# Performance work log

Measured on AMD Instinct MI355X. Metric: run time of the kernel, lower is better.

Reference implementation:

```python
import jax, jax.numpy as jnp
import numpy as np

B, T, C_IN, DIM, NFFT, HOP = 8, 1024, 256, 512, 1024, 256
NOUT = NFFT // 2 + 1
BB_DIL = (1, 1, 2, 2, 4, 4, 8, 8)
RES_DIL = (1, 3, 5)
N_RES = 3


def conv1d(x, w, b, dilation=1, groups=1, padding=0):
    # x: (B,C,T), w: (O, I/groups, K)
    y = jax.lax.conv_general_dilated(
        x, w, window_strides=(1,), padding=[(padding, padding)],
        rhs_dilation=(dilation,), dimension_numbers=('NCH', 'OIH', 'NCH'),
        feature_group_count=groups)
    return y + b[None, :, None]


def layernorm(x, g, b, eps=1e-6):
    m = jnp.mean(x, -1, keepdims=True)
    v = jnp.mean((x - m) ** 2, -1, keepdims=True)
    return (x - m) * jax.lax.rsqrt(v + eps) * g + b


def istft(spec, window):
    # spec: (B, F, Tf) complex, center=True, hann window, win_length=n_fft
    Bsz, F_, Tf = spec.shape
    frames = jnp.fft.irfft(spec, n=NFFT, axis=1)            # (B, n_fft, Tf)
    frames = jnp.transpose(frames, (0, 2, 1)) * window       # (B, Tf, n_fft)
    L = NFFT + HOP * (Tf - 1)
    idx = jnp.arange(Tf)[:, None] * HOP + jnp.arange(NFFT)[None, :]  # (Tf, n_fft)
    y = jnp.zeros((Bsz, L), frames.dtype).at[:, idx].add(frames)
    env = jnp.zeros((L,), window.dtype).at[idx].add(
        jnp.broadcast_to(window ** 2, (Tf, NFFT)))
    y = y / jnp.where(env > 1e-11, env, 1.0)
    start = NFFT // 2
    return y[:, start:start + HOP * (Tf - 1)]


def setup_inputs() -> dict:
    key = jax.random.key(0)
    ks = iter(jax.random.split(key, 64))
    r = lambda *s: jax.random.normal(next(ks), s, jnp.float32) * 0.02
    return {
        'x': jax.random.normal(next(ks), (B, T, C_IN), jnp.float32),
        'conv_in_w': r(DIM, C_IN, 7), 'conv_in_b': r(DIM),
        'skip_w': r(DIM, C_IN, 1), 'skip_b': r(DIM),
        'bb_dw_w': r(8, DIM, 1, 7), 'bb_dw_b': r(8, DIM),
        'bb_ln_g': jnp.ones((8, DIM), jnp.float32), 'bb_ln_b': jnp.zeros((8, DIM), jnp.float32),
        'bb_pw1_w': r(8, 4 * DIM, DIM), 'bb_pw1_b': r(8, 4 * DIM),
        'bb_pw2_w': r(8, DIM, 4 * DIM), 'bb_pw2_b': r(8, DIM),
        'bb_gamma': jnp.full((8, DIM), 1e-6, jnp.float32),
        'res_w1': r(N_RES, 3, DIM, DIM, 3), 'res_b1': r(N_RES, 3, DIM),
        'res_w2': r(N_RES, 3, DIM, DIM, 3), 'res_b2': r(N_RES, 3, DIM),
        'ln_g': jnp.ones((DIM,), jnp.float32), 'ln_b': jnp.zeros((DIM,), jnp.float32),
        'mag_w1': r(DIM, DIM), 'mag_b1': r(DIM),
        'mag_w2': r(NOUT, DIM), 'mag_b2': r(NOUT),
        'ph_w': r(NOUT, DIM), 'ph_b': r(NOUT),
        'cumsum_w': jnp.linspace(0.05, 0.4, NOUT, dtype=jnp.float32)[None, :],
        'window': (0.5 - 0.5 * jnp.cos(2.0 * jnp.pi * jnp.arange(NFFT) / NFFT)).astype(jnp.float32),
    }


def reference(x, conv_in_w, conv_in_b, skip_w, skip_b,
              bb_dw_w, bb_dw_b, bb_ln_g, bb_ln_b,
              bb_pw1_w, bb_pw1_b, bb_pw2_w, bb_pw2_b, bb_gamma,
              res_w1, res_b1, res_w2, res_b2,
              ln_g, ln_b, mag_w1, mag_b1, mag_w2, mag_b2,
              ph_w, ph_b, cumsum_w, window):
    # (B,T,C) -> (B,C,T)
    h = jnp.transpose(x, (0, 2, 1))
    skip = conv1d(h, skip_w, skip_b)                     # (B,DIM,T)
    hp = jnp.pad(h, ((0, 0), (0, 0), (3, 3)), mode='reflect')
    h = conv1d(hp, conv_in_w, conv_in_b)                 # kernel 7, pad 0 -> (B,DIM,T)
    # ConvNeXt backbone
    for i, d in enumerate(BB_DIL):
        res = h
        pad = (7 + (d - 1) * 6) // 2
        y = conv1d(h, bb_dw_w[i], bb_dw_b[i], dilation=d, groups=DIM, padding=pad)
        y = jnp.transpose(y, (0, 2, 1))                  # (B,T,DIM)
        y = layernorm(y, bb_ln_g[i], bb_ln_b[i])
        y = jax.nn.gelu(y @ bb_pw1_w[i].T + bb_pw1_b[i], approximate=False)
        y = y @ bb_pw2_w[i].T + bb_pw2_b[i]
        y = bb_gamma[i] * y
        h = res + jnp.transpose(y, (0, 2, 1))
    h = h + skip                                         # same length T
    # Residual dilated conv stacks
    for i in range(N_RES):
        for j, d in enumerate(RES_DIL):
            y = conv1d(h, res_w1[i, j], res_b1[i, j], dilation=d, padding=d)
            y = jax.nn.leaky_relu(y, 0.1)
            y = conv1d(y, res_w2[i, j], res_b2[i, j], padding=1)
            h = h + y
    h = jnp.transpose(h, (0, 2, 1))                      # (B,T,DIM)
    h = layernorm(h, ln_g, ln_b)
    # magnitude head
    m = jax.nn.gelu(h @ mag_w1.T + mag_b1, approximate=False)
    log_mag = m @ mag_w2.T + mag_b2
    mag = jnp.exp(jnp.clip(log_mag, -10.0, 10.0))        # (B,T,NOUT)
    # instantaneous-frequency phase head
    inst = jnp.tanh(h @ ph_w.T + ph_b) * jnp.pi
    phase = jnp.cumsum(inst * cumsum_w, axis=1)
    phase = jnp.remainder(phase + jnp.pi, 2.0 * jnp.pi) - jnp.pi
    # synthesize
    spec = jax.lax.complex(mag * jnp.cos(phase), mag * jnp.sin(phase))
    spec = jnp.transpose(spec, (0, 2, 1))                # (B,F,T)
    return istft(spec, window)
```

## Files before the change

kernel.cpp:

```cpp
#include <hip/hip_runtime.h>
#include <math.h>

constexpr int Bv = 8, Tv = 1024, DIMC = 512, NOUTC = 513;
constexpr int Mrows = Bv * 1024;
constexpr int LDS_S = 1056;
constexpr float PI_F = 3.14159265358979323846f;
constexpr float TWOPI_F = 6.28318530717958647692f;

struct TapInfo { int n; int off[7]; };
struct PtrTable { _Float16* h[36]; };

enum { BND_NONE = 0, BND_ZERO, BND_REFLECT };

typedef _Float16 half8v __attribute__((ext_vector_type(8)));
typedef _Float16 half4v __attribute__((ext_vector_type(4)));
typedef float f32x4 __attribute__((ext_vector_type(4)));

__device__ __forceinline__ void gld_lds16(const void* g, void* l) {
  __builtin_amdgcn_global_load_lds(
      (const __attribute__((address_space(1))) unsigned int*)g,
      (__attribute__((address_space(3))) unsigned int*)l, 16, 0, 0);
}

enum { MEPI_GELU_H = 0, MEPI_GAMMARES };

template<int EPI, int TN, int KS>
__global__ __launch_bounds__(256)
void mfma_gemm(const _Float16* __restrict__ A, int lda,
               const _Float16* __restrict__ W, int K,
               const float* __restrict__ bias,
               const float* __restrict__ aux,
               float* __restrict__ hio,
               _Float16* __restrict__ Ch,
               int N, int ldc)
{
  constexpr int NFR = TN / 32;
  __shared__ _Float16 sA[2][KS * 128 * 32];
  __shared__ _Float16 sB[2][KS * TN * 32];
  const int m0 = blockIdx.x * 128;
  const int n0 = blockIdx.y * TN;
  const int tid = threadIdx.x;
  const int wid = tid >> 6, lane = tid & 63;
  const int wr = wid >> 1, wc = wid & 1;
  const int fr = lane & 15, fq = lane >> 4;

  f32x4 acc[4][NFR] = {};

  const int rbase = tid >> 2;
  const int kwS = (((tid & 3) ^ ((tid >> 3) & 3)) << 3);
  const int nst = K / (32 * KS);
  const int fqS = fq ^ ((fr >> 1) & 3);
  const int aBase = (wr * 64 + fr) * 32 + fqS * 8;
  const int bBase = (wc * (TN / 2) + fr) * 32 + fqS * 8;

  const _Float16* arow[2];
  #pragma unroll
  for (int s = 0; s < 2; ++s)
    arow[s] = A + (size_t)(m0 + s * 64 + rbase) * lda + kwS;

  auto STAGE = [&](int st, int buf) {
    #pragma unroll
    for (int ks = 0; ks < KS; ++ks) {
      const int k0 = (st * KS + ks) << 5;
      #pragma unroll
      for (int s = 0; s < 2; ++s)
        gld_lds16(arow[s] + k0,
                  (char*)&sA[buf][0] + ks * 8192 + s * 4096 + wid * 1024);
      #pragma unroll
      for (int s = 0; s < TN / 64; ++s) {
        size_t bo = (size_t)(n0 + s * 64 + rbase) * K + kwS + k0;
        gld_lds16(W + bo,
                  (char*)&sB[buf][0] + ks * (TN * 64) + s * 4096 + wid * 1024);
      }
    }
  };
  auto COMPUTE = [&](int buf) {
    #pragma unroll
    for (int ks = 0; ks < KS; ++ks) {
      half8v aF[4], bF[NFR];
      #pragma unroll
      for (int i = 0; i < 4; ++i)
        aF[i] = *(const half8v*)&sA[buf][ks * 4096 + aBase + i * 512];
      #pragma unroll
      for (int j = 0; j < NFR; ++j)
        bF[j] = *(const half8v*)&sB[buf][ks * (TN * 32) + bBase + j * 512];
      #pragma unroll
      for (int i = 0; i < 4; ++i)
        #pragma unroll
        for (int j = 0; j < NFR; ++j)
          acc[i][j] = __builtin_amdgcn_mfma_f32_16x16x32_f16(aF[i], bF[j], acc[i][j], 0, 0, 0);
    }
  };

  STAGE(0, 0);
  __syncthreads();
  int cur = 0;
  for (int st = 0; st < nst; ++st) {
    if (st + 1 < nst) STAGE(st + 1, cur ^ 1);
    COMPUTE(cur);
    __syncthreads();
    cur ^= 1;
  }

  #pragma unroll
  for (int j = 0; j < NFR; ++j) {
    const int n = n0 + wc * (TN / 2) + j * 16 + fr;
    const float bj = bias[n];
    const float gj = (EPI == MEPI_GAMMARES) ? aux[n] : 0.f;
    #pragma unroll
    for (int i = 0; i < 4; ++i) {
      const int mB = m0 + wr * 64 + i * 16 + fq * 4;
      #pragma unroll
      for (int r = 0; r < 4; ++r) {
        const int m = mB + r;
        float v = acc[i][j][r] + bj;
        if (EPI == MEPI_GELU_H) {
          v = 0.5f * v * (1.f + erff(v * 0.70710678118654752f));
          Ch[(size_t)m * ldc + n] = (_Float16)v;
        } else {
          hio[(size_t)m * ldc + n] += gj * v;
        }
      }
    }
  }
}

enum { SEPI_F32 = 0, SEPI_LEAKY_SPLIT, SEPI_ADDRES_SPLIT,
       SEPI_GELU_SPLIT, SEPI_EXPCLIP, SEPI_TANHCW };

template<int EPI, int BND, int TN>
__global__ __launch_bounds__(256)
void mfma_gemm_split(const _Float16* __restrict__ Ah, const _Float16* __restrict__ Al, int lda,
                     const _Float16* __restrict__ Wh, const _Float16* __restrict__ Wl, int K,
                     const float* __restrict__ bias,
                     const float* __restrict__ aux,
                     float* __restrict__ hio,
                     float* __restrict__ Cf,
                     _Float16* __restrict__ Chh, _Float16* __restrict__ Chl,
                     int N, int ldc,
                     const _Float16* __restrict__ zpage,
                     TapInfo taps)
{
  constexpr int NFR = TN / 32;
  __shared__ _Float16 sAh[2][128 * 32];
  __shared__ _Float16 sAl[2][128 * 32];
  __shared__ _Float16 sBh[2][TN * 32];
  __shared__ _Float16 sBl[2][TN * 32];
  const int m0 = blockIdx.x * 128;
  const int n0 = blockIdx.y * TN;
  const int tid = threadIdx.x;
  const int wid = tid >> 6, lane = tid & 63;
  const int wr = wid >> 1, wc = wid & 1;
  const int fr = lane & 15, fq = lane >> 4;

  f32x4 acc[4][NFR] = {};

  const int t0 = m0 & (Tv - 1);
  const int rbase = tid >> 2;
  const int kwS = (((tid & 3) ^ ((tid >> 3) & 3)) << 3);
  const int nkc = K >> 5;
  const int NT = taps.n * nkc;
  const int fqS = fq ^ ((fr >> 1) & 3);
  const int aBase = (wr * 64 + fr) * 32 + fqS * 8;
  const int bBase = (wc * (TN / 2) + fr) * 32 + fqS * 8;

  auto STAGE = [&](int st, int buf) {
    int tap = (taps.n == 1) ? 0 : (st / nkc);
    int kc = st - tap * nkc;
    const int k0 = kc << 5;
    const int off = (BND == BND_NONE) ? 0 : taps.off[tap];
    const _Float16* Wth = Wh + (size_t)tap * N * K;
    const _Float16* Wtl = Wl + (size_t)tap * N * K;
    #pragma unroll
    for (int s = 0; s < 2; ++s) {
      int t = t0 + s * 64 + rbase + off;
      bool valid = true;
      if (BND == BND_REFLECT) t = (t < 0) ? -t : (t >= Tv ? 2 * Tv - 2 - t : t);
      else if (BND == BND_ZERO) valid = (t >= 0) && (t < Tv);
      size_t ro = (size_t)(m0 - t0 + t) * lda + kwS + k0;
      const void* sh = valid ? (const void*)(Ah + ro) : (const void*)zpage;
      const void* sl = valid ? (const void*)(Al + ro) : (const void*)zpage;
      gld_lds16(sh, (char*)&sAh[buf][0] + s * 4096 + wid * 1024);
      gld_lds16(sl, (char*)&sAl[buf][0] + s * 4096 + wid * 1024);
    }
    #pragma unroll
    for (int s = 0; s < TN / 64; ++s) {
      size_t bo = (size_t)(n0 + s * 64 + rbase) * K + kwS + k0;
      gld_lds16(Wth + bo, (char*)&sBh[buf][0] + s * 4096 + wid * 1024);
      gld_lds16(Wtl + bo, (char*)&sBl[buf][0] + s * 4096 + wid * 1024);
    }
  };

  auto COMPUTE = [&](int buf) {
    half8v ah[4], al[4], bh[NFR], bl[NFR];
    #pragma unroll
    for (int i = 0; i < 4; ++i) {
      ah[i] = *(const half8v*)&sAh[buf][aBase + i * 512];
      al[i] = *(const half8v*)&sAl[buf][aBase + i * 512];
    }
    #pragma unroll
    for (int j = 0; j < NFR; ++j) {
      bh[j] = *(const half8v*)&sBh[buf][bBase + j * 512];
      bl[j] = *(const half8v*)&sBl[buf][bBase + j * 512];
    }
    #pragma unroll
    for (int i = 0; i < 4; ++i)
      #pragma unroll
      for (int j = 0; j < NFR; ++j) {
        acc[i][j] = __builtin_amdgcn_mfma_f32_16x16x32_f16(ah[i], bh[j], acc[i][j], 0, 0, 0);
        acc[i][j] = __builtin_amdgcn_mfma_f32_16x16x32_f16(ah[i], bl[j], acc[i][j], 0, 0, 0);
        acc[i][j] = __builtin_amdgcn_mfma_f32_16x16x32_f16(al[i], bh[j], acc[i][j], 0, 0, 0);
      }
  };

  STAGE(0, 0);
  __syncthreads();
  int cur = 0;
  for (int st = 0; st < NT; ++st) {
    if (st + 1 < NT) STAGE(st + 1, cur ^ 1);
    COMPUTE(cur);
    __syncthreads();
    cur ^= 1;
  }

  #pragma unroll
  for (int j = 0; j < NFR; ++j) {
    const int n = n0 + wc * (TN / 2) + j * 16 + fr;
    const bool nok = (n < N);
    const float bj = (nok && bias) ? bias[n] : 0.f;
    const float ax = (EPI == SEPI_TANHCW && nok) ? aux[n] : 0.f;
    #pragma unroll
    for (int i = 0; i < 4; ++i) {
      const int mB = m0 + wr * 64 + i * 16 + fq * 4;
      #pragma unroll
      for (int r = 0; r < 4; ++r) {
        const int m = mB + r;
        float v = acc[i][j][r] + bj;
        if (!nok) continue;
        if (EPI == SEPI_F32) {
          Cf[(size_t)m * ldc + n] = v;
        } else if (EPI == SEPI_GELU_SPLIT) {
          v = 0.5f * v * (1.f + erff(v * 0.70710678118654752f));
          _Float16 hi = (_Float16)v;
          Chh[(size_t)m * ldc + n] = hi;
          Chl[(size_t)m * ldc + n] = (_Float16)(v - (float)hi);
        } else if (EPI == SEPI_EXPCLIP) {
          Cf[(size_t)m * ldc + n] = expf(fminf(fmaxf(v, -10.f), 10.f));
        } else if (EPI == SEPI_TANHCW) {
          Cf[(size_t)m * ldc + n] = tanhf(v) * PI_F * ax;
        }
      }
    }
  }
}

enum { REPI_LEAKY = 0, REPI_ADDRES };

template<int EPI>
__global__ __launch_bounds__(256)
void res_gemm(const _Float16* __restrict__ Ah, const _Float16* __restrict__ Al,
              const _Float16* __restrict__ Wh, const _Float16* __restrict__ Wl,
              const float* __restrict__ bias,
              float* __restrict__ hio,
              _Float16* __restrict__ Chh, _Float16* __restrict__ Chl,
              const _Float16* __restrict__ zpage,
              int d)
{
  __shared__ _Float16 sAh_[160 * 32];
  __shared__ _Float16 sAl_[160 * 32];
  __shared__ _Float16 sB_[3 * 2 * 64 * 32];
  const int m0 = blockIdx.x * 128;
  const int n0 = blockIdx.y * 64;
  const int tid = threadIdx.x;
  const int wid = tid >> 6, lane = tid & 63;
  const int wr = wid >> 1, wc = wid & 1;
  const int fr = lane & 15, fq = lane >> 4;
  const int t0 = m0 & (Tv - 1);

  f32x4 acc[4][2] = {};
  const int offs[3] = {-d, 0, d};

  for (int kc = 0; kc < 16; ++kc) {
    const int k0h = kc << 5;
    #pragma unroll
    for (int it = 0; it < 5; ++it) {
      int cb = it * 4 + wid;
      int half = (cb >= 10) ? 1 : 0;
      int rb = (cb - half * 10) * 16;
      int row = rb + (lane >> 2);
      int slot_g = (lane & 3) ^ ((row >> 1) & 3);
      int t = t0 - 16 + row;
      bool valid = (t >= 0) && (t < Tv);
      const _Float16* srcb = half ? Al : Ah;
      const void* src = valid
          ? (const void*)(srcb + (size_t)(m0 - t0 + t) * DIMC + k0h + slot_g * 8)
          : (const void*)(zpage + slot_g * 8);
      void* dst = (char*)(half ? sAl_ : sAh_) + rb * 64;
      gld_lds16(src, dst);
    }
    #pragma unroll
    for (int it = 0; it < 6; ++it) {
      int cb = it * 4 + wid;
      int tap = cb >> 3;
      int r2 = cb & 7;
      int half = r2 >> 2;
      int rb = (r2 & 3) * 16;
      int row = rb + (lane >> 2);
      int slot_g = (lane & 3) ^ ((row >> 1) & 3);
      const _Float16* srcb = (half ? Wl : Wh) + (size_t)tap * 512 * 512
                           + (size_t)(n0 + row) * 512 + k0h + slot_g * 8;
      void* dst = (char*)sB_ + ((size_t)(tap * 2 + half) * 64 + rb) * 64;
      gld_lds16(srcb, dst);
    }
    __syncthreads();

    #pragma unroll
    for (int tap = 0; tap < 3; ++tap) {
      const int off = offs[tap];
      half8v ah[4], al[4], bh[2], bl[2];
      #pragma unroll
      for (int i = 0; i < 4; ++i) {
        int rA = wr * 64 + i * 16 + fr + off + 16;
        int ab = rA * 64 + ((fq ^ ((rA >> 1) & 3)) * 16);
        ah[i] = *(const half8v*)((const char*)sAh_ + ab);
        al[i] = *(const half8v*)((const char*)sAl_ + ab);
      }
      #pragma unroll
      for (int j = 0; j < 2; ++j) {
        int rB = wc * 32 + j * 16 + fr;
        int bb = rB * 64 + ((fq ^ ((rB >> 1) & 3)) * 16);
        bh[j] = *(const half8v*)((const char*)sB_ + (tap * 2 + 0) * 4096 + bb);
        bl[j] = *(const half8v*)((const char*)sB_ + (tap * 2 + 1) * 4096 + bb);
      }
      #pragma unroll
      for (int i = 0; i < 4; ++i)
        #pragma unroll
        for (int j = 0; j < 2; ++j) {
          acc[i][j] = __builtin_amdgcn_mfma_f32_16x16x32_f16(ah[i], bh[j], acc[i][j], 0, 0, 0);
          acc[i][j] = __builtin_amdgcn_mfma_f32_16x16x32_f16(ah[i], bl[j], acc[i][j], 0, 0, 0);
          acc[i][j] = __builtin_amdgcn_mfma_f32_16x16x32_f16(al[i], bh[j], acc[i][j], 0, 0, 0);
        }
    }
    __syncthreads();
  }

  #pragma unroll
  for (int j = 0; j < 2; ++j) {
    const int n = n0 + wc * 32 + j * 16 + fr;
    const float bj = bias[n];
    #pragma unroll
    for (int i = 0; i < 4; ++i) {
      const int mB = m0 + wr * 64 + i * 16 + fq * 4;
      #pragma unroll
      for (int r = 0; r < 4; ++r) {
        const int m = mB + r;
        float v = acc[i][j][r] + bj;
        if (EPI == REPI_LEAKY) {
          v = (v > 0.f) ? v : 0.1f * v;
          _Float16 hi = (_Float16)v;
          Chh[(size_t)m * DIMC + n] = hi;
          Chl[(size_t)m * DIMC + n] = (_Float16)(v - (float)hi);
        } else {
          float nh = hio[(size_t)m * DIMC + n] + v;
          hio[(size_t)m * DIMC + n] = nh;
          _Float16 hi = (_Float16)nh;
          Chh[(size_t)m * DIMC + n] = hi;
          Chl[(size_t)m * DIMC + n] = (_Float16)(nh - (float)hi);
        }
      }
    }
  }
}

__global__ __launch_bounds__(256)
void convin_gemm(const _Float16* __restrict__ Ah, const _Float16* __restrict__ Al,
                 const _Float16* __restrict__ Wh, const _Float16* __restrict__ Wl,
                 const float* __restrict__ bias,
                 float* __restrict__ Cf)
{
  __shared__ _Float16 sAh_[160 * 32];
  __shared__ _Float16 sAl_[160 * 32];
  __shared__ _Float16 sB_[7 * 2 * 64 * 32];
  const int m0 = blockIdx.x * 128;
  const int n0 = blockIdx.y * 64;
  const int tid = threadIdx.x;
  const int wid = tid >> 6, lane = tid & 63;
  const int wr = wid >> 1, wc = wid & 1;
  const int fr = lane & 15, fq = lane >> 4;
  const int t0 = m0 & (Tv - 1);

  f32x4 acc[4][2] = {};

  for (int kc = 0; kc < 8; ++kc) {
    const int k0h = kc << 5;
    #pragma unroll
    for (int it = 0; it < 5; ++it) {
      int cb = it * 4 + wid;
      int half = (cb >= 10) ? 1 : 0;
      int rb = (cb - half * 10) * 16;
      int row = rb + (lane >> 2);
      int slot_g = (lane & 3) ^ ((row >> 1) & 3);
      int t = t0 - 16 + row;
      t = (t < 0) ? -t : (t >= Tv ? 2 * Tv - 2 - t : t);
      const _Float16* srcb = half ? Al : Ah;
      const void* src = srcb + (size_t)(m0 - t0 + t) * 256 + k0h + slot_g * 8;
      void* dst = (char*)(half ? sAl_ : sAh_) + rb * 64;
      gld_lds16(src, dst);
    }
    #pragma unroll
    for (int it = 0; it < 14; ++it) {
      int cb = it * 4 + wid;
      int tap = cb >> 3;
      int r2 = cb & 7;
      int half = r2 >> 2;
      int rb = (r2 & 3) * 16;
      int row = rb + (lane >> 2);
      int slot_g = (lane & 3) ^ ((row >> 1) & 3);
      const _Float16* srcb = (half ? Wl : Wh) + (size_t)tap * 512 * 256
                           + (size_t)(n0 + row) * 256 + k0h + slot_g * 8;
      void* dst = (char*)sB_ + ((size_t)(tap * 2 + half) * 64 + rb) * 64;
      gld_lds16(srcb, dst);
    }
    __syncthreads();

    #pragma unroll
    for (int tap = 0; tap < 7; ++tap) {
      const int off = tap - 3;
      half8v ah[4], al[4], bh[2], bl[2];
      #pragma unroll
      for (int i = 0; i < 4; ++i) {
        int rA = wr * 64 + i * 16 + fr + off + 16;
        int ab = rA * 64 + ((fq ^ ((rA >> 1) & 3)) * 16);
        ah[i] = *(const half8v*)((const char*)sAh_ + ab);
        al[i] = *(const half8v*)((const char*)sAl_ + ab);
      }
      #pragma unroll
      for (int j = 0; j < 2; ++j) {
        int rB = wc * 32 + j * 16 + fr;
        int bb = rB * 64 + ((fq ^ ((rB >> 1) & 3)) * 16);
        bh[j] = *(const half8v*)((const char*)sB_ + (tap * 2 + 0) * 4096 + bb);
        bl[j] = *(const half8v*)((const char*)sB_ + (tap * 2 + 1) * 4096 + bb);
      }
      #pragma unroll
      for (int i = 0; i < 4; ++i)
        #pragma unroll
        for (int j = 0; j < 2; ++j) {
          acc[i][j] = __builtin_amdgcn_mfma_f32_16x16x32_f16(ah[i], bh[j], acc[i][j], 0, 0, 0);
          acc[i][j] = __builtin_amdgcn_mfma_f32_16x16x32_f16(ah[i], bl[j], acc[i][j], 0, 0, 0);
          acc[i][j] = __builtin_amdgcn_mfma_f32_16x16x32_f16(al[i], bh[j], acc[i][j], 0, 0, 0);
        }
    }
    __syncthreads();
  }

  #pragma unroll
  for (int j = 0; j < 2; ++j) {
    const int n = n0 + wc * 32 + j * 16 + fr;
    const float bj = bias[n];
    #pragma unroll
    for (int i = 0; i < 4; ++i) {
      const int mB = m0 + wr * 64 + i * 16 + fq * 4;
      #pragma unroll
      for (int r = 0; r < 4; ++r) {
        const int m = mB + r;
        Cf[(size_t)m * DIMC + n] = acc[i][j][r] + bj;
      }
    }
  }
}

__global__ __launch_bounds__(256)
void dwln(const float* __restrict__ h, const float* __restrict__ wt,
          const float* __restrict__ bias, const float* __restrict__ g,
          const float* __restrict__ be, _Float16* __restrict__ out, int d)
{
  int wid = threadIdx.x >> 6, lane = threadIdx.x & 63;
  int m = (blockIdx.x << 2) + wid;
  int t = m & (Tv - 1);
  int bT = m - t;
  int c0 = lane * 8;
  float acc[8];
  {
    float4 b0 = *(const float4*)&bias[c0];
    float4 b1 = *(const float4*)&bias[c0 + 4];
    acc[0] = b0.x; acc[1] = b0.y; acc[2] = b0.z; acc[3] = b0.w;
    acc[4] = b1.x; acc[5] = b1.y; acc[6] = b1.z; acc[7] = b1.w;
  }
  #pragma unroll
  for (int k = 0; k < 7; ++k) {
    int tt = t + (k - 3) * d;
    if (tt < 0 || tt >= Tv) continue;
    const float* hp = &h[(size_t)(bT + tt) * DIMC + c0];
    float4 v0 = *(const float4*)hp;
    float4 v1 = *(const float4*)(hp + 4);
    const float* wp = &wt[k * DIMC + c0];
    float4 w0 = *(const float4*)wp;
    float4 w1 = *(const float4*)(wp + 4);
    float hv[8] = {v0.x, v0.y, v0.z, v0.w, v1.x, v1.y, v1.z, v1.w};
    float wv[8] = {w0.x, w0.y, w0.z, w0.w, w1.x, w1.y, w1.z, w1.w};
    #pragma unroll
    for (int q = 0; q < 8; ++q)
      acc[q] = fmaf(hv[q], wv[q], acc[q]);
  }
  float sum = 0.f;
  #pragma unroll
  for (int q = 0; q < 8; ++q) sum += acc[q];
  #pragma unroll
  for (int o = 32; o > 0; o >>= 1) sum += __shfl_xor(sum, o);
  float mean = sum * (1.f / 512.f);
  float vs = 0.f;
  #pragma unroll
  for (int q = 0; q < 8; ++q) { float dd = acc[q] - mean; vs = fmaf(dd, dd, vs); }
  #pragma unroll
  for (int o = 32; o > 0; o >>= 1) vs += __shfl_xor(vs, o);
  float rstd = rsqrtf(vs * (1.f / 512.f) + 1e-6f);
  float4 g0 = *(const float4*)&g[c0];
  float4 g1 = *(const float4*)&g[c0 + 4];
  float4 e0 = *(const float4*)&be[c0];
  float4 e1 = *(const float4*)&be[c0 + 4];
  float gv[8] = {g0.x, g0.y, g0.z, g0.w, g1.x, g1.y, g1.z, g1.w};
  float ev[8] = {e0.x, e0.y, e0.z, e0.w, e1.x, e1.y, e1.z, e1.w};
  half8v ov;
  #pragma unroll
  for (int q = 0; q < 8; ++q)
    ov[q] = (_Float16)((acc[q] - mean) * rstd * gv[q] + ev[q]);
  *(half8v*)&out[(size_t)m * DIMC + c0] = ov;
}

__global__ __launch_bounds__(256)
void repack_dw(const float* __restrict__ in, float* __restrict__ out)
{
  int idx = blockIdx.x * 256 + threadIdx.x;
  if (idx >= 8 * 512 * 7) return;
  int l = idx / 3584;
  int r = idx - l * 3584;
  int c = r / 7, k = r - c * 7;
  out[l * 3584 + k * 512 + c] = in[idx];
}

__global__ __launch_bounds__(256)
void lnorm_split(const float* __restrict__ in, const float* __restrict__ g,
                 const float* __restrict__ be,
                 _Float16* __restrict__ ohi, _Float16* __restrict__ olo)
{
  int wid = threadIdx.x >> 6, lane = threadIdx.x & 63;
  int m = (blockIdx.x << 2) + wid;
  int c0 = lane * 8;
  const float* row = in + (size_t)m * DIMC + c0;
  float4 v0 = *(const float4*)row;
  float4 v1 = *(const float4*)(row + 4);
  float acc[8] = {v0.x, v0.y, v0.z, v0.w, v1.x, v1.y, v1.z, v1.w};
  float sum = 0.f;
  #pragma unroll
  for (int q = 0; q < 8; ++q) sum += acc[q];
  #pragma unroll
  for (int o = 32; o > 0; o >>= 1) sum += __shfl_xor(sum, o);
  float mean = sum * (1.f / 512.f);
  float vs = 0.f;
  #pragma unroll
  for (int q = 0; q < 8; ++q) { float dd = acc[q] - mean; vs = fmaf(dd, dd, vs); }
  #pragma unroll
  for (int o = 32; o > 0; o >>= 1) vs += __shfl_xor(vs, o);
  float rstd = rsqrtf(vs * (1.f / 512.f) + 1e-6f);
  float4 g0 = *(const float4*)&g[c0];
  float4 g1 = *(const float4*)&g[c0 + 4];
  float4 e0 = *(const float4*)&be[c0];
  float4 e1 = *(const float4*)&be[c0 + 4];
  float gv[8] = {g0.x, g0.y, g0.z, g0.w, g1.x, g1.y, g1.z, g1.w};
  float ev[8] = {e0.x, e0.y, e0.z, e0.w, e1.x, e1.y, e1.z, e1.w};
  half8v hv, lv;
  #pragma unroll
  for (int q = 0; q < 8; ++q) {
    float v = (acc[q] - mean) * rstd * gv[q] + ev[q];
    _Float16 hi = (_Float16)v;
    hv[q] = hi; lv[q] = (_Float16)(v - (float)hi);
  }
  *(half8v*)&ohi[(size_t)m * DIMC + c0] = hv;
  *(half8v*)&olo[(size_t)m * DIMC + c0] = lv;
}

__global__ __launch_bounds__(256)
void add_split(float* __restrict__ a, const float* __restrict__ b,
               _Float16* __restrict__ hi, _Float16* __restrict__ lo, int n)
{
  int i = (blockIdx.x * 256 + threadIdx.x) * 4;
  if (i >= n) return;
  float4 va = *(const float4*)&a[i];
  float4 vb = *(const float4*)&b[i];
  float v[4] = {va.x + vb.x, va.y + vb.y, va.z + vb.z, va.w + vb.w};
  *(float4*)&a[i] = make_float4(v[0], v[1], v[2], v[3]);
  half4v h, l;
  #pragma unroll
  for (int q = 0; q < 4; ++q) {
    _Float16 hh = (_Float16)v[q];
    h[q] = hh; l[q] = (_Float16)(v[q] - (float)hh);
  }
  *(half4v*)&hi[i] = h;
  *(half4v*)&lo[i] = l;
}

__global__ __launch_bounds__(256)
void cvt_split(const float* __restrict__ in, _Float16* __restrict__ hi,
               _Float16* __restrict__ lo, int n)
{
  int i = (blockIdx.x * 256 + threadIdx.x) * 4;
  if (i >= n) return;
  float4 vv = *(const float4*)&in[i];
  float v[4] = {vv.x, vv.y, vv.z, vv.w};
  half4v h, l;
  #pragma unroll
  for (int q = 0; q < 4; ++q) {
    _Float16 hh = (_Float16)v[q];
    h[q] = hh; l[q] = (_Float16)(v[q] - (float)hh);
  }
  *(half4v*)&hi[i] = h;
  *(half4v*)&lo[i] = l;
}

__global__ __launch_bounds__(256)
void cvt_split_pad(const float* __restrict__ in, _Float16* __restrict__ hi,
                   _Float16* __restrict__ lo, int rows, int cols, int padRows)
{
  int i = blockIdx.x * 256 + threadIdx.x;
  if (i >= padRows * cols) return;
  int r = i / cols;
  float v = (r < rows) ? in[i] : 0.f;
  _Float16 h = (_Float16)v;
  hi[i] = h; lo[i] = (_Float16)(v - (float)h);
}

__global__ __launch_bounds__(256)
void cvt_h(const float* __restrict__ in, _Float16* __restrict__ out, int n)
{
  int i = (blockIdx.x * 256 + threadIdx.x) * 4;
  if (i >= n) return;
  float4 v = *(const float4*)&in[i];
  half4v h;
  h[0] = (_Float16)v.x; h[1] = (_Float16)v.y;
  h[2] = (_Float16)v.z; h[3] = (_Float16)v.w;
  *(half4v*)&out[i] = h;
}

__global__ __launch_bounds__(256)
void repack_split(const float* __restrict__ in, _Float16* __restrict__ hi,
                  _Float16* __restrict__ lo, int O, int C, int KT)
{
  int idx = blockIdx.x * 256 + threadIdx.x;
  if (idx >= O * C) return;
  int o = idx / C, c = idx - o * C;
  for (int k = 0; k < KT; ++k) {
    float v = in[((size_t)o * C + c) * KT + k];
    _Float16 h = (_Float16)v;
    size_t dst = ((size_t)k * O + o) * C + c;
    hi[dst] = h; lo[dst] = (_Float16)(v - (float)h);
  }
}

__global__ __launch_bounds__(256)
void repack_all(const float* __restrict__ res_w1, const float* __restrict__ res_w2,
                PtrTable pt)
{
  int blk = blockIdx.x;
  int conv = blk >> 10;
  int idx = ((blk & 1023) << 8) + threadIdx.x;
  int o = idx >> 9, c = idx & 511;
  const float* src = (conv < 9) ? (res_w1 + (size_t)conv * 786432)
                                : (res_w2 + (size_t)(conv - 9) * 786432);
  _Float16* hi = pt.h[conv * 2];
  _Float16* lo = pt.h[conv * 2 + 1];
  #pragma unroll
  for (int k = 0; k < 3; ++k) {
    float v = src[((size_t)o * 512 + c) * 3 + k];
    _Float16 hh = (_Float16)v;
    size_t dst = ((size_t)k * 512 + o) * 512 + c;
    hi[dst] = hh; lo[dst] = (_Float16)(v - (float)hh);
  }
}

__global__ __launch_bounds__(256)
void zero_fill16(_Float16* __restrict__ p)
{
  int i = threadIdx.x * 8;
  #pragma unroll
  for (int q = 0; q < 8; ++q) p[i + q] = (_Float16)0.f;
}

__global__ __launch_bounds__(256)
void build_basis_split(const float* __restrict__ window,
                       _Float16* __restrict__ bhi, _Float16* __restrict__ blo)
{
  int n = blockIdx.x;
  float wn = window[n];
  const float invN = 1.f / 1024.f;
  for (int j = threadIdx.x; j < LDS_S; j += 256) {
    float coef = 0.f;
    if (j < 513) {
      int k = j;
      if (k == 0)        coef = invN;
      else if (k == 512) coef = (n & 1) ? -invN : invN;
      else {
        int r = (k * n) & 1023;
        coef = 2.f * invN * cosf(TWOPI_F * (float)r * (1.f / 1024.f));
      }
    } else if (j < 1026) {
      int k = j - 513;
      if (k != 0 && k != 512) {
        int r = (k * n) & 1023;
        coef = -2.f * invN * sinf(TWOPI_F * (float)r * (1.f / 1024.f));
      }
    }
    float v = coef * wn;
    _Float16 hi = (_Float16)v;
    bhi[(size_t)n * LDS_S + j] = hi;
    blo[(size_t)n * LDS_S + j] = (_Float16)(v - (float)hi);
  }
}

__global__ __launch_bounds__(256)
void scan_part(const float* __restrict__ dph, float* __restrict__ psum)
{
  int b = blockIdx.x, fg = blockIdx.y;
  int w = threadIdx.x >> 6, lane = threadIdx.x & 63;
  int tc = blockIdx.z * 4 + w;
  int f = fg * 64 + lane;
  if (f >= NOUTC) return;
  const float* p = dph + (size_t)(b * Tv + tc * 32) * NOUTC + f;
  float s = 0.f;
  #pragma unroll 8
  for (int j = 0; j < 32; ++j) s += p[(size_t)j * NOUTC];
  psum[((size_t)b * 32 + tc) * 520 + f] = s;
}

__global__ __launch_bounds__(256)
void scan_off(float* __restrict__ psum)
{
  int idx = blockIdx.x * 256 + threadIdx.x;
  if (idx >= 8 * NOUTC) return;
  int b = idx / NOUTC, f = idx - b * NOUTC;
  float run = 0.f;
  for (int tc = 0; tc < 32; ++tc) {
    size_t o = ((size_t)b * 32 + tc) * 520 + f;
    float v = psum[o];
    psum[o] = run;
    run += v;
  }
}

__global__ __launch_bounds__(256)
void scan_emit(const float* __restrict__ dph, const float* __restrict__ mag,
               const float* __restrict__ psum,
               _Float16* __restrict__ Shi, _Float16* __restrict__ Slo)
{
  int b = blockIdx.x, fg = blockIdx.y;
  int w = threadIdx.x >> 6, lane = threadIdx.x & 63;
  int tc = blockIdx.z * 4 + w;
  int f = fg * 64 + lane;
  if (f >= NOUTC) return;
  float run = psum[((size_t)b * 32 + tc) * 520 + f];
  const size_t base = (size_t)(b * Tv + tc * 32) * NOUTC + f;
  for (int j = 0; j < 32; ++j) {
    run += dph[base + (size_t)j * NOUTC];
    float r = fmodf(run + PI_F, TWOPI_F);
    if (r < 0.f) r += TWOPI_F;
    float wph = r - PI_F;
    float mg = mag[base + (size_t)j * NOUTC];
    float sn, cs;
    sincosf(wph, &sn, &cs);
    size_t mrow = (size_t)(b * Tv + tc * 32 + j) * LDS_S;
    float vc = mg * cs, vs2 = mg * sn;
    _Float16 hc = (_Float16)vc, hs = (_Float16)vs2;
    Shi[mrow + f] = hc;        Slo[mrow + f] = (_Float16)(vc - (float)hc);
    Shi[mrow + 513 + f] = hs;  Slo[mrow + 513 + f] = (_Float16)(vs2 - (float)hs);
  }
}

__global__ __launch_bounds__(256)
void pad_S(_Float16* __restrict__ Shi, _Float16* __restrict__ Slo)
{
  int idx = blockIdx.x * 256 + threadIdx.x;
  if (idx >= Mrows * 30) return;
  int m = idx / 30, c = 1026 + idx % 30;
  Shi[(size_t)m * LDS_S + c] = (_Float16)0.f;
  Slo[(size_t)m * LDS_S + c] = (_Float16)0.f;
}

__global__ __launch_bounds__(256)
void ola(const float* __restrict__ frames, const float* __restrict__ window,
         float* __restrict__ out)
{
  int idx = blockIdx.x * 256 + threadIdx.x;
  if (idx >= Bv * 261888) return;
  int b = idx / 261888;
  int i = idx - b * 261888;
  int l = i + 512;
  int tmax = l >> 8; if (tmax > 1023) tmax = 1023;
  int tmin = (l >= 1023) ? ((l - 1023 + 255) >> 8) : 0;
  float acc = 0.f, env = 0.f;
  for (int t = tmin; t <= tmax; ++t) {
    int n = l - (t << 8);
    acc += frames[(size_t)(b * Tv + t) * 1024 + n];
    float wv = window[n];
    env = fmaf(wv, wv, env);
  }
  out[idx] = acc / (env > 1e-11f ? env : 1.f);
}

extern "C" void kernel_launch(void* const* d_in, const int* in_sizes, int n_in,
                              void* d_out, int out_size, void* d_ws, size_t ws_size,
                              hipStream_t stream)
{
  const float* x         = (const float*)d_in[0];
  const float* conv_in_w = (const float*)d_in[1];
  const float* conv_in_b = (const float*)d_in[2];
  const float* skip_w    = (const float*)d_in[3];
  const float* skip_b    = (const float*)d_in[4];
  const float* bb_dw_w   = (const float*)d_in[5];
  const float* bb_dw_b   = (const float*)d_in[6];
  const float* bb_ln_g   = (const float*)d_in[7];
  const float* bb_ln_b   = (const float*)d_in[8];
  const float* bb_pw1_w  = (const float*)d_in[9];
  const float* bb_pw1_b  = (const float*)d_in[10];
  const float* bb_pw2_w  = (const float*)d_in[11];
  const float* bb_pw2_b  = (const float*)d_in[12];
  const float* bb_gamma  = (const float*)d_in[13];
  const float* res_w1    = (const float*)d_in[14];
  const float* res_b1    = (const float*)d_in[15];
  const float* res_w2    = (const float*)d_in[16];
  const float* res_b2    = (const float*)d_in[17];
  const float* ln_g      = (const float*)d_in[18];
  const float* ln_b      = (const float*)d_in[19];
  const float* mag_w1    = (const float*)d_in[20];
  const float* mag_b1    = (const float*)d_in[21];
  const float* mag_w2    = (const float*)d_in[22];
  const float* mag_b2    = (const float*)d_in[23];
  const float* ph_w      = (const float*)d_in[24];
  const float* ph_b      = (const float*)d_in[25];
  const float* cumsum_w  = (const float*)d_in[26];
  const float* window    = (const float*)d_in[27];
  float* out = (float*)d_out;
  float* ws  = (float*)d_ws;

  float* w_h     = ws;
  float* w_skip  = ws + 4194304;
  float* w_t4    = ws + 8388608;
  float* w_mag   = ws + 12582912;
  float* w_dph   = ws + 16785408;
  float* w_basis = ws + 20987904;
  float* w_big   = ws + 22069248;
  _Float16* t3h  = (_Float16*)w_big;
  _Float16* h_hi = (_Float16*)w_big;
  _Float16* h_lo = h_hi + 4194304;
  _Float16* y_hi = h_hi + 8388608;
  _Float16* y_lo = h_hi + 12582912;
  _Float16* Shi  = (_Float16*)w_big;
  _Float16* Slo  = Shi + 8650752;
  float* w_frames= w_h;

  _Float16* t2h  = (_Float16*)(ws + 30720000);
  _Float16* x_hi = (_Float16*)(ws + 32817152);
  _Float16* x_lo = (_Float16*)(ws + 33865728);
  _Float16* wA_hi= (_Float16*)(ws + 34914304);
  _Float16* wA_lo= (_Float16*)(ws + 35438592);
  _Float16* wB_hi= (_Float16*)(ws + 35962880);
  _Float16* wB_lo= (_Float16*)(ws + 36487168);
  _Float16* zpg  = (_Float16*)(ws + 37011456);
  float* w_psum  = ws + 37012480;
  float* w_dwT   = ws + 37145600;

  _Float16* wpw1h = (_Float16*)w_t4;
  _Float16* wpw2h = (_Float16*)w_mag;

  static const size_t slotOffF[18] = {
    8388608, 9175040, 9961472, 10747904, 11534336,
    12582912, 13369344, 14155776, 14942208, 15728640,
    16785408, 17571840, 18358272, 19144704, 19931136,
    32817152, 33603584,
    30720000
  };
  PtrTable pt;
  for (int cv = 0; cv < 18; ++cv) {
    _Float16* hi = (_Float16*)(ws + slotOffF[cv]);
    pt.h[cv * 2] = hi;
    pt.h[cv * 2 + 1] = hi + 786432;
  }

  _Float16* lshi = (_Float16*)w_skip;
  _Float16* lslo = lshi + 4194304;
  _Float16* t4hi = (_Float16*)w_t4;
  _Float16* t4lo = t4hi + 4194304;
  _Float16* m1hi = t2h;
  _Float16* m1lo = t2h + 262144;
  _Float16* m2hi = t2h + 524288;
  _Float16* m2lo = t2h + 851968;
  _Float16* phhi = t2h + 1179648;
  _Float16* phlo = t2h + 1507328;
  _Float16* bhi  = (_Float16*)w_basis;
  _Float16* blo  = bhi + 1081344;

  dim3 blk(256);
  TapInfo tp1{1, {0}};

  zero_fill16<<<dim3(1), blk, 0, stream>>>(zpg);
  cvt_split<<<dim3(8192 * 256 / 4 / 256), blk, 0, stream>>>(x, x_hi, x_lo, 8192 * 256);
  cvt_h<<<dim3(8388608 / 4 / 256), blk, 0, stream>>>(bb_pw1_w, wpw1h, 8388608);
  cvt_h<<<dim3(8388608 / 4 / 256), blk, 0, stream>>>(bb_pw2_w, wpw2h, 8388608);
  repack_dw<<<dim3(112), blk, 0, stream>>>(bb_dw_w, w_dwT);

  repack_split<<<dim3(512 * 256 / 256), blk, 0, stream>>>(conv_in_w, wA_hi, wA_lo, 512, 256, 7);
  convin_gemm<<<dim3(64, 8), blk, 0, stream>>>(
      x_hi, x_lo, wA_hi, wA_lo, conv_in_b, w_h);
  repack_split<<<dim3(512 * 256 / 256), blk, 0, stream>>>(skip_w, wB_hi, wB_lo, 512, 256, 1);
  mfma_gemm_split<SEPI_F32, BND_NONE, 64><<<dim3(64, 8), blk, 0, stream>>>(
      x_hi, x_lo, 256, wB_hi, wB_lo, 256, skip_b, nullptr, nullptr, w_skip, nullptr, nullptr,
      512, 512, zpg, tp1);

  const int dil[8] = {1, 1, 2, 2, 4, 4, 8, 8};
  for (int i = 0; i < 8; ++i) {
    dwln<<<dim3(2048), blk, 0, stream>>>(w_h, w_dwT + i * 3584, bb_dw_b + i * 512,
                                         bb_ln_g + i * 512, bb_ln_b + i * 512, t2h, dil[i]);
    mfma_gemm<MEPI_GELU_H, 128, 1><<<dim3(64, 16), blk, 0, stream>>>(
        t2h, 512, wpw1h + (size_t)i * 2048 * 512, 512, bb_pw1_b + i * 2048,
        nullptr, nullptr, t3h, 2048, 2048);
    mfma_gemm<MEPI_GAMMARES, 64, 2><<<dim3(64, 8), blk, 0, stream>>>(
        t3h, 2048, wpw2h + (size_t)i * 512 * 2048, 2048, bb_pw2_b + i * 512,
        bb_gamma + i * 512, w_h, nullptr, 512, 512);
  }
  add_split<<<dim3(4194304 / 4 / 256), blk, 0, stream>>>(w_h, w_skip, h_hi, h_lo, 4194304);

  repack_all<<<dim3(18 * 1024), blk, 0, stream>>>(res_w1, res_w2, pt);

  const int rdil[3] = {1, 3, 5};
  for (int i = 0; i < 3; ++i)
    for (int j = 0; j < 3; ++j) {
      int d = rdil[j];
      int idx = i * 3 + j;
      res_gemm<REPI_LEAKY><<<dim3(64, 8), blk, 0, stream>>>(
          h_hi, h_lo, pt.h[idx * 2], pt.h[idx * 2 + 1],
          res_b1 + idx * 512, nullptr, y_hi, y_lo, zpg, d);
      res_gemm<REPI_ADDRES><<<dim3(64, 8), blk, 0, stream>>>(
          y_hi, y_lo, pt.h[(9 + idx) * 2], pt.h[(9 + idx) * 2 + 1],
          res_b2 + idx * 512, w_h, h_hi, h_lo, zpg, 1);
    }

  lnorm_split<<<dim3(2048), blk, 0, stream>>>(w_h, ln_g, ln_b, lshi, lslo);

  cvt_split<<<dim3(262144 / 4 / 256), blk, 0, stream>>>(mag_w1, m1hi, m1lo, 262144);
  cvt_split_pad<<<dim3(640 * 512 / 256), blk, 0, stream>>>(mag_w2, m2hi, m2lo, 513, 512, 640);
  cvt_split_pad<<<dim3(640 * 512 / 256), blk, 0, stream>>>(ph_w, phhi, phlo, 513, 512, 640);

  mfma_gemm_split<SEPI_GELU_SPLIT, BND_NONE, 64><<<dim3(64, 8), blk, 0, stream>>>(
      lshi, lslo, 512, m1hi, m1lo, 512, mag_b1, nullptr, nullptr, nullptr,
      t4hi, t4lo, 512, 512, zpg, tp1);
  mfma_gemm_split<SEPI_EXPCLIP, BND_NONE, 64><<<dim3(64, 10), blk, 0, stream>>>(
      t4hi, t4lo, 512, m2hi, m2lo, 512, mag_b2, nullptr, nullptr, w_mag,
      nullptr, nullptr, 513, 513, zpg, tp1);
  mfma_gemm_split<SEPI_TANHCW, BND_NONE, 64><<<dim3(64, 10), blk, 0, stream>>>(
      lshi, lslo, 512, phhi, phlo, 512, ph_b, cumsum_w, nullptr, w_dph,
      nullptr, nullptr, 513, 513, zpg, tp1);

  build_basis_split<<<dim3(1024), blk, 0, stream>>>(window, bhi, blo);
  pad_S<<<dim3((Mrows * 30 + 255) / 256), blk, 0, stream>>>(Shi, Slo);
  scan_part<<<dim3(8, 9, 8), blk, 0, stream>>>(w_dph, w_psum);
  scan_off<<<dim3(17), blk, 0, stream>>>(w_psum);
  scan_emit<<<dim3(8, 9, 8), blk, 0, stream>>>(w_dph, w_mag, w_psum, Shi, Slo);
  mfma_gemm_split<SEPI_F32, BND_NONE, 128><<<dim3(64, 8), blk, 0, stream>>>(
      Shi, Slo, LDS_S, bhi, blo, LDS_S, nullptr, nullptr, nullptr, w_frames,
      nullptr, nullptr, 1024, 1024, zpg, tp1);
  ola<<<dim3((Bv * 261888 + 255) / 256), blk, 0, stream>>>(w_frames, window, out);
}
```

Before: 1.839 ms.

## Double-buffer res_gemm LDS staging and keep residual only as fp16 hi/lo

```diff
diff --git a/kernel.cpp b/kernel.cpp
--- a/kernel.cpp
+++ b/kernel.cpp
@@ -261,14 +261,15 @@
 void res_gemm(const _Float16* __restrict__ Ah, const _Float16* __restrict__ Al,
               const _Float16* __restrict__ Wh, const _Float16* __restrict__ Wl,
               const float* __restrict__ bias,
-              float* __restrict__ hio,
+              const _Float16* __restrict__ prevHi,
+              const _Float16* __restrict__ prevLo,
               _Float16* __restrict__ Chh, _Float16* __restrict__ Chl,
               const _Float16* __restrict__ zpage,
               int d)
 {
-  __shared__ _Float16 sAh_[160 * 32];
-  __shared__ _Float16 sAl_[160 * 32];
-  __shared__ _Float16 sB_[3 * 2 * 64 * 32];
+  __shared__ _Float16 sAh_[2][160 * 32];
+  __shared__ _Float16 sAl_[2][160 * 32];
+  __shared__ _Float16 sB_[2][3 * 2 * 64 * 32];
   const int m0 = blockIdx.x * 128;
   const int n0 = blockIdx.y * 64;
   const int tid = threadIdx.x;
@@ -280,7 +281,7 @@
   f32x4 acc[4][2] = {};
   const int offs[3] = {-d, 0, d};
 
-  for (int kc = 0; kc < 16; ++kc) {
+  auto STAGE = [&](int kc, int buf) {
     const int k0h = kc << 5;
     #pragma unroll
     for (int it = 0; it < 5; ++it) {
@@ -295,7 +296,7 @@
       const void* src = valid
           ? (const void*)(srcb + (size_t)(m0 - t0 + t) * DIMC + k0h + slot_g * 8)
           : (const void*)(zpage + slot_g * 8);
-      void* dst = (char*)(half ? sAl_ : sAh_) + rb * 64;
+      void* dst = (char*)(half ? &sAl_[buf][0] : &sAh_[buf][0]) + rb * 64;
       gld_lds16(src, dst);
     }
     #pragma unroll
@@ -309,11 +310,12 @@
       int slot_g = (lane & 3) ^ ((row >> 1) & 3);
       const _Float16* srcb = (half ? Wl : Wh) + (size_t)tap * 512 * 512
                            + (size_t)(n0 + row) * 512 + k0h + slot_g * 8;
-      void* dst = (char*)sB_ + ((size_t)(tap * 2 + half) * 64 + rb) * 64;
+      void* dst = (char*)&sB_[buf][0] + ((size_t)(tap * 2 + half) * 64 + rb) * 64;
       gld_lds16(srcb, dst);
     }
-    __syncthreads();
-
+  };
+
+  auto COMPUTE = [&](int buf) {
     #pragma unroll
     for (int tap = 0; tap < 3; ++tap) {
       const int off = offs[tap];
@@ -322,15 +324,15 @@
       for (int i = 0; i < 4; ++i) {
         int rA = wr * 64 + i * 16 + fr + off + 16;
         int ab = rA * 64 + ((fq ^ ((rA >> 1) & 3)) * 16);
-        ah[i] = *(const half8v*)((const char*)sAh_ + ab);
-        al[i] = *(const half8v*)((const char*)sAl_ + ab);
+        ah[i] = *(const half8v*)((const char*)&sAh_[buf][0] + ab);
+        al[i] = *(const half8v*)((const char*)&sAl_[buf][0] + ab);
       }
       #pragma unroll
       for (int j = 0; j < 2; ++j) {
         int rB = wc * 32 + j * 16 + fr;
         int bb = rB * 64 + ((fq ^ ((rB >> 1) & 3)) * 16);
-        bh[j] = *(const half8v*)((const char*)sB_ + (tap * 2 + 0) * 4096 + bb);
-        bl[j] = *(const half8v*)((const char*)sB_ + (tap * 2 + 1) * 4096 + bb);
+        bh[j] = *(const half8v*)((const char*)&sB_[buf][0] + (tap * 2 + 0) * 4096 + bb);
+        bl[j] = *(const half8v*)((const char*)&sB_[buf][0] + (tap * 2 + 1) * 4096 + bb);
       }
       #pragma unroll
       for (int i = 0; i < 4; ++i)
@@ -341,7 +343,16 @@
           acc[i][j] = __builtin_amdgcn_mfma_f32_16x16x32_f16(al[i], bh[j], acc[i][j], 0, 0, 0);
         }
     }
+  };
+
+  STAGE(0, 0);
+  __syncthreads();
+  int cur = 0;
+  for (int kc = 0; kc < 16; ++kc) {
+    if (kc + 1 < 16) STAGE(kc + 1, cur ^ 1);
+    COMPUTE(cur);
     __syncthreads();
+    cur ^= 1;
   }
 
   #pragma unroll
@@ -361,11 +372,12 @@
           Chh[(size_t)m * DIMC + n] = hi;
           Chl[(size_t)m * DIMC + n] = (_Float16)(v - (float)hi);
         } else {
-          float nh = hio[(size_t)m * DIMC + n] + v;
-          hio[(size_t)m * DIMC + n] = nh;
+          size_t o = (size_t)m * DIMC + n;
+          float ph = (float)prevHi[o] + (float)prevLo[o];
+          float nh = ph + v;
           _Float16 hi = (_Float16)nh;
-          Chh[(size_t)m * DIMC + n] = hi;
-          Chl[(size_t)m * DIMC + n] = (_Float16)(nh - (float)hi);
+          Chh[o] = hi;
+          Chl[o] = (_Float16)(nh - (float)hi);
         }
       }
     }
@@ -539,17 +551,18 @@
 }
 
 __global__ __launch_bounds__(256)
-void lnorm_split(const float* __restrict__ in, const float* __restrict__ g,
-                 const float* __restrict__ be,
+void lnorm_split(const _Float16* __restrict__ ihi, const _Float16* __restrict__ ilo,
+                 const float* __restrict__ g, const float* __restrict__ be,
                  _Float16* __restrict__ ohi, _Float16* __restrict__ olo)
 {
   int wid = threadIdx.x >> 6, lane = threadIdx.x & 63;
   int m = (blockIdx.x << 2) + wid;
   int c0 = lane * 8;
-  const float* row = in + (size_t)m * DIMC + c0;
-  float4 v0 = *(const float4*)row;
-  float4 v1 = *(const float4*)(row + 4);
-  float acc[8] = {v0.x, v0.y, v0.z, v0.w, v1.x, v1.y, v1.z, v1.w};
+  half8v ha = *(const half8v*)&ihi[(size_t)m * DIMC + c0];
+  half8v hb = *(const half8v*)&ilo[(size_t)m * DIMC + c0];
+  float acc[8];
+  #pragma unroll
+  for (int q = 0; q < 8; ++q) acc[q] = (float)ha[q] + (float)hb[q];
   float sum = 0.f;
   #pragma unroll
   for (int q = 0; q < 8; ++q) sum += acc[q];
@@ -580,7 +593,7 @@
 }
 
 __global__ __launch_bounds__(256)
-void add_split(float* __restrict__ a, const float* __restrict__ b,
+void add_split(const float* __restrict__ a, const float* __restrict__ b,
                _Float16* __restrict__ hi, _Float16* __restrict__ lo, int n)
 {
   int i = (blockIdx.x * 256 + threadIdx.x) * 4;
@@ -588,7 +601,6 @@
   float4 va = *(const float4*)&a[i];
   float4 vb = *(const float4*)&b[i];
   float v[4] = {va.x + vb.x, va.y + vb.y, va.z + vb.z, va.w + vb.w};
-  *(float4*)&a[i] = make_float4(v[0], v[1], v[2], v[3]);
   half4v h, l;
   #pragma unroll
   for (int q = 0; q < 4; ++q) {
@@ -936,13 +948,13 @@
       int idx = i * 3 + j;
       res_gemm<REPI_LEAKY><<<dim3(64, 8), blk, 0, stream>>>(
           h_hi, h_lo, pt.h[idx * 2], pt.h[idx * 2 + 1],
-          res_b1 + idx * 512, nullptr, y_hi, y_lo, zpg, d);
+          res_b1 + idx * 512, nullptr, nullptr, y_hi, y_lo, zpg, d);
       res_gemm<REPI_ADDRES><<<dim3(64, 8), blk, 0, stream>>>(
           y_hi, y_lo, pt.h[(9 + idx) * 2], pt.h[(9 + idx) * 2 + 1],
-          res_b2 + idx * 512, w_h, h_hi, h_lo, zpg, 1);
-    }
-
-  lnorm_split<<<dim3(2048), blk, 0, stream>>>(w_h, ln_g, ln_b, lshi, lslo);
+          res_b2 + idx * 512, h_hi, h_lo, h_hi, h_lo, zpg, 1);
+    }
+
+  lnorm_split<<<dim3(2048), blk, 0, stream>>>(h_hi, h_lo, ln_g, ln_b, lshi, lslo);
 
   cvt_split<<<dim3(262144 / 4 / 256), blk, 0, stream>>>(mag_w1, m1hi, m1lo, 262144);
   cvt_split_pad<<<dim3(640 * 512 / 256), blk, 0, stream>>>(mag_w2, m2hi, m2lo, 513, 512, 640);
```

New measurement: 2.126 ms. 1.16x slower.
